# Performance work log

Measured on AMD Instinct MI355X. Metric: run time of the kernel, lower is better.

The kernel has to match this reference:

```python
import jax, jax.numpy as jnp
import numpy as np

NUM_EXPERTS = 16
HIDDEN = 2048
INTER = 768
TOP_K = 8
N_TOKENS = 4096


def setup_inputs() -> dict:
    key = jax.random.key(0)
    k1, k2, k3, k4, k5 = jax.random.split(key, 5)
    hidden_states = jax.random.normal(k1, (N_TOKENS, HIDDEN), dtype=jnp.float32)
    routing_weights = jax.random.uniform(k2, (N_TOKENS, NUM_EXPERTS), dtype=jnp.float32)
    router_indices = jax.random.randint(k3, (N_TOKENS, TOP_K), 0, NUM_EXPERTS)
    gate_up_proj = jax.random.normal(k4, (NUM_EXPERTS, HIDDEN, 2 * INTER), dtype=jnp.float32) * 0.02
    down_proj = jax.random.normal(k5, (NUM_EXPERTS, INTER, HIDDEN), dtype=jnp.float32) * 0.02
    return {
        "hidden_states": hidden_states,
        "routing_weights": routing_weights,
        "router_indices": router_indices,
        "gate_up_proj": gate_up_proj,
        "down_proj": down_proj,
    }


def reference(hidden_states, routing_weights, router_indices, gate_up_proj, down_proj):
    # Training-path MoE math (permute + grouped GEMM + SwiGLU + grouped GEMM +
    # unpermute/combine), expressed as dense per-expert GEMMs combined with a
    # sparse combine matrix built from the top-k router indices.
    n_tokens, hidden = hidden_states.shape
    n_experts = gate_up_proj.shape[0]
    # selected_probs[t, k] = routing_weights[t, router_indices[t, k]]
    selected_probs = jnp.take_along_axis(routing_weights, router_indices, axis=1)  # [N, K]
    # combine[t, e] = sum over k of selected_probs where router_indices[t,k] == e
    rows = jnp.arange(n_tokens)[:, None]
    combine = jnp.zeros((n_tokens, n_experts), dtype=hidden_states.dtype)
    combine = combine.at[rows, router_indices].add(selected_probs)  # [N, E]
    # grouped GEMM #1 (gate_up): [N,H] x [E,H,2I] -> [E,N,2I]
    gate_up = jnp.einsum("nh,ehf->enf", hidden_states, gate_up_proj)
    gate, up = jnp.split(gate_up, 2, axis=-1)
    inter = jax.nn.silu(gate) * up  # SwiGLU, [E,N,I]
    # grouped GEMM #2 (down): [E,N,I] x [E,I,H] -> [E,N,H]
    expert_out = jnp.einsum("eni,eih->enh", inter, down_proj)
    # combine / unpermute: weighted sum over selected experts
    out = jnp.einsum("enh,ne->nh", expert_out, combine)  # [N, H]
    return out
```

## Files before the change

kernel.cpp:

```cpp
#include <hip/hip_runtime.h>
#include <hip/hip_bf16.h>

#define NE 16
#define H  2048
#define I  768
#define TK 8
#define NT 4096
#define BM 128
#define BK 64

typedef unsigned short u16;
typedef unsigned int u32;
typedef __attribute__((ext_vector_type(8))) short bf16x8;
typedef __attribute__((ext_vector_type(4))) float f32x4;

__device__ __forceinline__ u16 f2bf(float f) {
    u32 u = __float_as_uint(f);
    u32 r = (u + 0x7fffu + ((u >> 16) & 1u)) >> 16;
    return (u16)r;
}

__device__ __forceinline__ void gload16(const void* g, void* l) {
    __builtin_amdgcn_global_load_lds(
        (const __attribute__((address_space(1))) unsigned int*)g,
        (__attribute__((address_space(3))) unsigned int*)l, 16, 0, 0);
}

__global__ void route_kernel(const float* __restrict__ rw, const int* __restrict__ ridx,
                             int* __restrict__ cnt, int* __restrict__ tok_cap,
                             float* __restrict__ wt_cap) {
    int t = blockIdx.x * 256 + threadIdx.x;
    if (t >= NT) return;
    int idx[TK];
#pragma unroll
    for (int k = 0; k < TK; k++) idx[k] = ridx[t * TK + k];
#pragma unroll
    for (int e = 0; e < NE; e++) {
        int mult = 0;
#pragma unroll
        for (int k = 0; k < TK; k++) mult += (idx[k] == e) ? 1 : 0;
        if (mult) {
            float w = (float)mult * rw[t * NE + e];
            int slot = atomicAdd(&cnt[e], 1);
            tok_cap[e * NT + slot] = t;
            wt_cap[e * NT + slot] = w;
        }
    }
}

__global__ void prefix_kernel(const int* __restrict__ cnt, int* __restrict__ base) {
    if (threadIdx.x == 0 && blockIdx.x == 0) {
        int s = 0;
        for (int e = 0; e < NE; e++) { base[e] = s; s += cnt[e]; }
        base[NE] = s;
    }
}

__global__ void compact_kernel(const int* __restrict__ cnt, const int* __restrict__ base,
                               const int* __restrict__ tok_cap, const float* __restrict__ wt_cap,
                               int* __restrict__ tok, float* __restrict__ wt) {
    int i = blockIdx.x * 256 + threadIdx.x;
    int e = i >> 12, s = i & 4095;
    if (e < NE && s < cnt[e]) {
        tok[base[e] + s] = tok_cap[e * NT + s];
        wt[base[e] + s]  = wt_cap[e * NT + s];
    }
}

__global__ void cvt_hs(const float4* __restrict__ in, uint4* __restrict__ out, int n) {
    int i = blockIdx.x * 256 + threadIdx.x;
    if (i >= n) return;
    float4 a = in[i * 2], b = in[i * 2 + 1];
    uint4 o;
    o.x = (u32)f2bf(a.x) | ((u32)f2bf(a.y) << 16);
    o.y = (u32)f2bf(a.z) | ((u32)f2bf(a.w) << 16);
    o.z = (u32)f2bf(b.x) | ((u32)f2bf(b.y) << 16);
    o.w = (u32)f2bf(b.z) | ((u32)f2bf(b.w) << 16);
    out[i] = o;
}

__global__ void transpose_cvt(const float* __restrict__ in, u16* __restrict__ out,
                              int K, int N) {
    __shared__ float tile[64][65];
    const float* src = in + (size_t)blockIdx.z * K * N;
    u16* dst = out + (size_t)blockIdx.z * (size_t)K * N;
    int n0 = blockIdx.x * 64, k0 = blockIdx.y * 64;
    int tc = threadIdx.x & 63, tr = threadIdx.x >> 6;
    for (int r = tr; r < 64; r += 4)
        tile[r][tc] = src[(size_t)(k0 + r) * N + n0 + tc];
    __syncthreads();
    for (int r = tr; r < 64; r += 4)
        dst[(size_t)(n0 + r) * K + k0 + tc] = f2bf(tile[tc][r]);
}

__global__ __launch_bounds__(256, 2) void gemm1_kernel(
    const u16* __restrict__ hsb, const u16* __restrict__ w1t, u16* __restrict__ inter,
    const int* __restrict__ tok, const int* __restrict__ cnt, const int* __restrict__ base) {
    int e = blockIdx.z, mt = blockIdx.y, nt = blockIdx.x;
    int cn = cnt[e];
    if (mt * BM >= cn) return;
    int b0 = base[e];

    __shared__ u16 lA[BM * BK];
    __shared__ u16 lB[BM * BK];

    int tid = threadIdx.x, lane = tid & 63, wv = tid >> 6;

    const u16* gA[4];
    const u16* gB[4];
#pragma unroll
    for (int i = 0; i < 4; i++) {
        int c = i * 256 + tid;
        int r = c >> 3, ko = (c & 7) * 8;
        int rg = mt * BM + r;
        int t = tok[b0 + min(rg, cn - 1)];
        gA[i] = hsb + (size_t)t * H + ko;
        int nrow = (r < 64) ? (nt * 64 + r) : (704 + nt * 64 + r);
        gB[i] = w1t + (size_t)e * 1536 * H + (size_t)nrow * H + ko;
    }
    u16* lAd[4];
    u16* lBd[4];
#pragma unroll
    for (int i = 0; i < 4; i++) {
        lAd[i] = lA + (i * 256 + wv * 64) * 8;
        lBd[i] = lB + (i * 256 + wv * 64) * 8;
    }

    f32x4 acc[2][8];
#pragma unroll
    for (int m = 0; m < 2; m++)
#pragma unroll
        for (int n = 0; n < 8; n++) acc[m][n] = (f32x4)0.0f;

    for (int kt = 0; kt < H / BK; ++kt) {
        __syncthreads();
#pragma unroll
        for (int i = 0; i < 4; i++) { gload16(gA[i], lAd[i]); gload16(gB[i], lBd[i]); }
#pragma unroll
        for (int i = 0; i < 4; i++) { gA[i] += BK; gB[i] += BK; }
        __syncthreads();
#pragma unroll
        for (int s = 0; s < 2; s++) {
            int kk = s * 32 + (lane >> 4) * 8;
            bf16x8 a0 = *(const bf16x8*)&lA[(wv * 32 + (lane & 15)) * BK + kk];
            bf16x8 a1 = *(const bf16x8*)&lA[(wv * 32 + 16 + (lane & 15)) * BK + kk];
#pragma unroll
            for (int n = 0; n < 8; n++) {
                bf16x8 b = *(const bf16x8*)&lB[(n * 16 + (lane & 15)) * BK + kk];
                acc[0][n] = __builtin_amdgcn_mfma_f32_16x16x32_bf16(a0, b, acc[0][n], 0, 0, 0);
                acc[1][n] = __builtin_amdgcn_mfma_f32_16x16x32_bf16(a1, b, acc[1][n], 0, 0, 0);
            }
        }
    }

    int jr = (lane >> 4) * 4, col = lane & 15;
#pragma unroll
    for (int m = 0; m < 2; m++)
#pragma unroll
        for (int j = 0; j < 4; j++) {
            int r = wv * 32 + m * 16 + jr + j;
            int rg = mt * BM + r;
            if (rg < cn) {
                size_t slot = (size_t)(b0 + rg);
#pragma unroll
                for (int n = 0; n < 4; n++) {
                    float g = acc[m][n][j];
                    float u = acc[m][n + 4][j];
                    float sv = g / (1.0f + __expf(-g)) * u;
                    inter[slot * I + nt * 64 + n * 16 + col] = f2bf(sv);
                }
            }
        }
}

__global__ __launch_bounds__(256, 2) void gemm2_kernel(
    const u16* __restrict__ inter, const u16* __restrict__ w2t, float* __restrict__ out,
    const int* __restrict__ tok, const float* __restrict__ wt,
    const int* __restrict__ cnt, const int* __restrict__ base) {
    int e = blockIdx.z, mt = blockIdx.y, nt = blockIdx.x;
    int cn = cnt[e];
    if (mt * BM >= cn) return;
    int b0 = base[e];

    __shared__ u16 lA[BM * BK];
    __shared__ u16 lB[BM * BK];

    int tid = threadIdx.x, lane = tid & 63, wv = tid >> 6;

    const u16* gA[4];
    const u16* gB[4];
#pragma unroll
    for (int i = 0; i < 4; i++) {
        int c = i * 256 + tid;
        int r = c >> 3, ko = (c & 7) * 8;
        gA[i] = inter + (size_t)(b0 + mt * BM + r) * I + ko;
        gB[i] = w2t + (size_t)e * H * I + (size_t)(nt * BM + r) * I + ko;
    }
    u16* lAd[4];
    u16* lBd[4];
#pragma unroll
    for (int i = 0; i < 4; i++) {
        lAd[i] = lA + (i * 256 + wv * 64) * 8;
        lBd[i] = lB + (i * 256 + wv * 64) * 8;
    }

    f32x4 acc[2][8];
#pragma unroll
    for (int m = 0; m < 2; m++)
#pragma unroll
        for (int n = 0; n < 8; n++) acc[m][n] = (f32x4)0.0f;

    for (int kt = 0; kt < I / BK; ++kt) {
        __syncthreads();
#pragma unroll
        for (int i = 0; i < 4; i++) { gload16(gA[i], lAd[i]); gload16(gB[i], lBd[i]); }
#pragma unroll
        for (int i = 0; i < 4; i++) { gA[i] += BK; gB[i] += BK; }
        __syncthreads();
#pragma unroll
        for (int s = 0; s < 2; s++) {
            int kk = s * 32 + (lane >> 4) * 8;
            bf16x8 a0 = *(const bf16x8*)&lA[(wv * 32 + (lane & 15)) * BK + kk];
            bf16x8 a1 = *(const bf16x8*)&lA[(wv * 32 + 16 + (lane & 15)) * BK + kk];
#pragma unroll
            for (int n = 0; n < 8; n++) {
                bf16x8 b = *(const bf16x8*)&lB[(n * 16 + (lane & 15)) * BK + kk];
                acc[0][n] = __builtin_amdgcn_mfma_f32_16x16x32_bf16(a0, b, acc[0][n], 0, 0, 0);
                acc[1][n] = __builtin_amdgcn_mfma_f32_16x16x32_bf16(a1, b, acc[1][n], 0, 0, 0);
            }
        }
    }

    int jr = (lane >> 4) * 4, col = lane & 15;
#pragma unroll
    for (int m = 0; m < 2; m++)
#pragma unroll
        for (int j = 0; j < 4; j++) {
            int r = wv * 32 + m * 16 + jr + j;
            int rg = mt * BM + r;
            if (rg < cn) {
                int t = tok[b0 + rg];
                float w = wt[b0 + rg];
                float* orow = out + (size_t)t * H + nt * BM;
#pragma unroll
                for (int n = 0; n < 8; n++)
                    atomicAdd(&orow[n * 16 + col], w * acc[m][n][j]);
            }
        }
}

extern "C" void kernel_launch(void* const* d_in, const int* in_sizes, int n_in,
                              void* d_out, int out_size, void* d_ws, size_t ws_size,
                              hipStream_t stream) {
    const float* hs  = (const float*)d_in[0];
    const float* rw  = (const float*)d_in[1];
    const int*   ri  = (const int*)d_in[2];
    const float* w1  = (const float*)d_in[3];
    const float* w2  = (const float*)d_in[4];
    float* out = (float*)d_out;

    char* ws = (char*)d_ws;
    size_t o = 0;
    auto alloc = [&](size_t bytes) { void* p = ws + o; o += (bytes + 255) & ~(size_t)255; return p; };
    u16*   hsb    = (u16*)alloc((size_t)NT * H * 2);
    u16*   w1t    = (u16*)alloc((size_t)NE * 1536 * H * 2);
    u16*   w2t    = (u16*)alloc((size_t)NE * H * I * 2);
    u16*   inter  = (u16*)alloc((size_t)(NT * TK + 256) * I * 2);
    int*   tokcap = (int*)alloc((size_t)NE * NT * 4);
    float* wtcap  = (float*)alloc((size_t)NE * NT * 4);
    int*   tok    = (int*)alloc((size_t)NT * TK * 4);
    float* wt     = (float*)alloc((size_t)NT * TK * 4);
    int*   cnt    = (int*)alloc(64);
    int*   base   = (int*)alloc(128);

    hipMemsetAsync(cnt, 0, 64, stream);
    hipMemsetAsync(out, 0, (size_t)NT * H * 4, stream);

    route_kernel<<<NT / 256, 256, 0, stream>>>(rw, ri, cnt, tokcap, wtcap);
    prefix_kernel<<<1, 64, 0, stream>>>(cnt, base);
    compact_kernel<<<NE * NT / 256, 256, 0, stream>>>(cnt, base, tokcap, wtcap, tok, wt);
    cvt_hs<<<(NT * H / 8 + 255) / 256, 256, 0, stream>>>((const float4*)hs, (uint4*)hsb, NT * H / 8);
    {
        dim3 g(1536 / 64, H / 64, NE);
        transpose_cvt<<<g, 256, 0, stream>>>(w1, w1t, H, 1536);
    }
    {
        dim3 g(H / 64, I / 64, NE);
        transpose_cvt<<<g, 256, 0, stream>>>(w2, w2t, I, H);
    }
    {
        dim3 g(12, 32, NE);
        gemm1_kernel<<<g, 256, 0, stream>>>(hsb, w1t, inter, tok, cnt, base);
    }
    {
        dim3 g(16, 32, NE);
        gemm2_kernel<<<g, 256, 0, stream>>>(inter, w2t, out, tok, wt, cnt, base);
    }
}
```

Before: 873.2 us.

## Replace atomic combine with bf16 expert output buffer and per-token gather reduction

```diff
diff --git a/kernel.cpp b/kernel.cpp
--- a/kernel.cpp
+++ b/kernel.cpp
@@ -58,12 +58,17 @@
 
 __global__ void compact_kernel(const int* __restrict__ cnt, const int* __restrict__ base,
                                const int* __restrict__ tok_cap, const float* __restrict__ wt_cap,
-                               int* __restrict__ tok, float* __restrict__ wt) {
+                               int* __restrict__ tok, float* __restrict__ wt,
+                               int* __restrict__ tjc, int* __restrict__ tslot) {
     int i = blockIdx.x * 256 + threadIdx.x;
     int e = i >> 12, s = i & 4095;
     if (e < NE && s < cnt[e]) {
-        tok[base[e] + s] = tok_cap[e * NT + s];
-        wt[base[e] + s]  = wt_cap[e * NT + s];
+        int t = tok_cap[e * NT + s];
+        int slot = base[e] + s;
+        tok[slot] = t;
+        wt[slot]  = wt_cap[e * NT + s];
+        int j = atomicAdd(&tjc[t], 1);
+        tslot[t * TK + j] = slot;
     }
 }
 
@@ -79,24 +84,30 @@
     out[i] = o;
 }
 
-__global__ void transpose_cvt(const float* __restrict__ in, u16* __restrict__ out,
+__global__ void transpose_cvt(const float* __restrict__ in, u32* __restrict__ out,
                               int K, int N) {
     __shared__ float tile[64][65];
     const float* src = in + (size_t)blockIdx.z * K * N;
-    u16* dst = out + (size_t)blockIdx.z * (size_t)K * N;
+    u32* dst = out + (size_t)blockIdx.z * (size_t)K * N / 2;
     int n0 = blockIdx.x * 64, k0 = blockIdx.y * 64;
     int tc = threadIdx.x & 63, tr = threadIdx.x >> 6;
     for (int r = tr; r < 64; r += 4)
         tile[r][tc] = src[(size_t)(k0 + r) * N + n0 + tc];
     __syncthreads();
-    for (int r = tr; r < 64; r += 4)
-        dst[(size_t)(n0 + r) * K + k0 + tc] = f2bf(tile[tc][r]);
+    int kp = threadIdx.x & 31, rr = threadIdx.x >> 5;
+    for (int r = rr; r < 64; r += 8) {
+        u32 v = (u32)f2bf(tile[kp * 2][r]) | ((u32)f2bf(tile[kp * 2 + 1][r]) << 16);
+        dst[(size_t)(n0 + r) * (K / 2) + k0 / 2 + kp] = v;
+    }
 }
 
 __global__ __launch_bounds__(256, 2) void gemm1_kernel(
     const u16* __restrict__ hsb, const u16* __restrict__ w1t, u16* __restrict__ inter,
     const int* __restrict__ tok, const int* __restrict__ cnt, const int* __restrict__ base) {
-    int e = blockIdx.z, mt = blockIdx.y, nt = blockIdx.x;
+    int bid = blockIdx.x;
+    int lid = (bid & 7) * (6144 / 8) + (bid >> 3);
+    int mt = lid & 31, r2 = lid >> 5;
+    int nt = r2 % 12, e = r2 / 12;
     int cn = cnt[e];
     if (mt * BM >= cn) return;
     int b0 = base[e];
@@ -173,11 +184,16 @@
         }
 }
 
+template <int MODE>
 __global__ __launch_bounds__(256, 2) void gemm2_kernel(
-    const u16* __restrict__ inter, const u16* __restrict__ w2t, float* __restrict__ out,
+    const u16* __restrict__ inter, const u16* __restrict__ w2t,
+    u16* __restrict__ eo, float* __restrict__ out,
     const int* __restrict__ tok, const float* __restrict__ wt,
     const int* __restrict__ cnt, const int* __restrict__ base) {
-    int e = blockIdx.z, mt = blockIdx.y, nt = blockIdx.x;
+    int bid = blockIdx.x;
+    int lid = (bid & 7) * (8192 / 8) + (bid >> 3);
+    int mt = lid & 31, r2 = lid >> 5;
+    int nt = r2 & 15, e = r2 >> 4;
     int cn = cnt[e];
     if (mt * BM >= cn) return;
     int b0 = base[e];
@@ -239,14 +255,49 @@
             int r = wv * 32 + m * 16 + jr + j;
             int rg = mt * BM + r;
             if (rg < cn) {
-                int t = tok[b0 + rg];
-                float w = wt[b0 + rg];
-                float* orow = out + (size_t)t * H + nt * BM;
-#pragma unroll
-                for (int n = 0; n < 8; n++)
-                    atomicAdd(&orow[n * 16 + col], w * acc[m][n][j]);
+                if (MODE == 0) {
+                    u16* row = eo + (size_t)(b0 + rg) * H + nt * BM;
+#pragma unroll
+                    for (int n = 0; n < 8; n++)
+                        row[n * 16 + col] = f2bf(acc[m][n][j]);
+                } else {
+                    int t = tok[b0 + rg];
+                    float w = wt[b0 + rg];
+                    float* orow = out + (size_t)t * H + nt * BM;
+#pragma unroll
+                    for (int n = 0; n < 8; n++)
+                        atomicAdd(&orow[n * 16 + col], w * acc[m][n][j]);
+                }
             }
         }
+}
+
+__global__ __launch_bounds__(256) void combine_kernel(
+    const u16* __restrict__ eo, const float* __restrict__ wt,
+    const int* __restrict__ tjc, const int* __restrict__ tslot,
+    float* __restrict__ out) {
+    int t = blockIdx.x;
+    int c = threadIdx.x * 8;
+    float acc[8];
+#pragma unroll
+    for (int i = 0; i < 8; i++) acc[i] = 0.0f;
+    int jc = tjc[t];
+    for (int j = 0; j < jc; j++) {
+        int slot = tslot[t * TK + j];
+        float w = wt[slot];
+        uint4 v = *(const uint4*)(eo + (size_t)slot * H + c);
+        acc[0] += w * __uint_as_float(v.x << 16);
+        acc[1] += w * __uint_as_float(v.x & 0xffff0000u);
+        acc[2] += w * __uint_as_float(v.y << 16);
+        acc[3] += w * __uint_as_float(v.y & 0xffff0000u);
+        acc[4] += w * __uint_as_float(v.z << 16);
+        acc[5] += w * __uint_as_float(v.z & 0xffff0000u);
+        acc[6] += w * __uint_as_float(v.w << 16);
+        acc[7] += w * __uint_as_float(v.w & 0xffff0000u);
+    }
+    float4* o = (float4*)(out + (size_t)t * H + c);
+    o[0] = make_float4(acc[0], acc[1], acc[2], acc[3]);
+    o[1] = make_float4(acc[4], acc[5], acc[6], acc[7]);
 }
 
 extern "C" void kernel_launch(void* const* d_in, const int* in_sizes, int n_in,
@@ -262,38 +313,43 @@
     char* ws = (char*)d_ws;
     size_t o = 0;
     auto alloc = [&](size_t bytes) { void* p = ws + o; o += (bytes + 255) & ~(size_t)255; return p; };
+    int*   tokcap = (int*)alloc((size_t)NE * NT * 4);
+    float* wtcap  = (float*)alloc((size_t)NE * NT * 4);
+    int*   tok    = (int*)alloc((size_t)NT * TK * 4);
+    float* wt     = (float*)alloc((size_t)NT * TK * 4);
+    int*   tjc    = (int*)alloc((size_t)NT * 4);
+    int*   tslot  = (int*)alloc((size_t)NT * TK * 4);
+    int*   cnt    = (int*)alloc(64);
+    int*   base   = (int*)alloc(128);
     u16*   hsb    = (u16*)alloc((size_t)NT * H * 2);
     u16*   w1t    = (u16*)alloc((size_t)NE * 1536 * H * 2);
     u16*   w2t    = (u16*)alloc((size_t)NE * H * I * 2);
     u16*   inter  = (u16*)alloc((size_t)(NT * TK + 256) * I * 2);
-    int*   tokcap = (int*)alloc((size_t)NE * NT * 4);
-    float* wtcap  = (float*)alloc((size_t)NE * NT * 4);
-    int*   tok    = (int*)alloc((size_t)NT * TK * 4);
-    float* wt     = (float*)alloc((size_t)NT * TK * 4);
-    int*   cnt    = (int*)alloc(64);
-    int*   base   = (int*)alloc(128);
+    u16*   eo     = (u16*)alloc((size_t)(NT * TK + 256) * H * 2);
+    const bool use_eo = (o <= ws_size);
 
     hipMemsetAsync(cnt, 0, 64, stream);
-    hipMemsetAsync(out, 0, (size_t)NT * H * 4, stream);
+    hipMemsetAsync(tjc, 0, (size_t)NT * 4, stream);
+    if (!use_eo)
+        hipMemsetAsync(out, 0, (size_t)NT * H * 4, stream);
 
     route_kernel<<<NT / 256, 256, 0, stream>>>(rw, ri, cnt, tokcap, wtcap);
     prefix_kernel<<<1, 64, 0, stream>>>(cnt, base);
-    compact_kernel<<<NE * NT / 256, 256, 0, stream>>>(cnt, base, tokcap, wtcap, tok, wt);
+    compact_kernel<<<NE * NT / 256, 256, 0, stream>>>(cnt, base, tokcap, wtcap, tok, wt, tjc, tslot);
     cvt_hs<<<(NT * H / 8 + 255) / 256, 256, 0, stream>>>((const float4*)hs, (uint4*)hsb, NT * H / 8);
     {
         dim3 g(1536 / 64, H / 64, NE);
-        transpose_cvt<<<g, 256, 0, stream>>>(w1, w1t, H, 1536);
+        transpose_cvt<<<g, 256, 0, stream>>>(w1, (u32*)w1t, H, 1536);
     }
     {
         dim3 g(H / 64, I / 64, NE);
-        transpose_cvt<<<g, 256, 0, stream>>>(w2, w2t, I, H);
-    }
-    {
-        dim3 g(12, 32, NE);
-        gemm1_kernel<<<g, 256, 0, stream>>>(hsb, w1t, inter, tok, cnt, base);
-    }
-    {
-        dim3 g(16, 32, NE);
-        gemm2_kernel<<<g, 256, 0, stream>>>(inter, w2t, out, tok, wt, cnt, base);
-    }
-}
+        transpose_cvt<<<g, 256, 0, stream>>>(w2, (u32*)w2t, I, H);
+    }
+    gemm1_kernel<<<6144, 256, 0, stream>>>(hsb, w1t, inter, tok, cnt, base);
+    if (use_eo) {
+        gemm2_kernel<0><<<8192, 256, 0, stream>>>(inter, w2t, eo, out, tok, wt, cnt, base);
+        combine_kernel<<<NT, 256, 0, stream>>>(eo, wt, tjc, tslot, out);
+    } else {
+        gemm2_kernel<1><<<8192, 256, 0, stream>>>(inter, w2t, eo, out, tok, wt, cnt, base);
+    }
+}
```

Measured after the change: 801.8 us. 8.2% less time.
